# Optimization experiments

Hardware: AMD Instinct MI355X
Metric: run time of the kernel (lower is better)

The kernel has to match this reference:

```python
import jax, jax.numpy as jnp
import numpy as np

N_NODES = 100000
N_EDGES = 1000000
NUM_FEATURES = 64
HIDDEN = 64
NUM_GRAPHS = 128


def setup_inputs() -> dict:
    key = jax.random.key(0)
    ks = jax.random.split(key, 12)
    x = jax.random.normal(ks[0], (N_NODES, NUM_FEATURES), dtype=jnp.float32)
    edge_index = jax.random.randint(ks[1], (2, N_EDGES), 0, N_NODES, dtype=jnp.int64)
    edge_weight = jax.random.uniform(ks[2], (N_EDGES,), dtype=jnp.float32)
    batch = jnp.sort(jax.random.randint(ks[3], (N_NODES,), 0, NUM_GRAPHS, dtype=jnp.int64))
    s1 = 1.0 / np.sqrt(NUM_FEATURES)
    s2 = 1.0 / np.sqrt(HIDDEN)
    # GraphConv layer 1: lin_rel (with bias) applied to aggregated msgs, lin_root (no bias)
    w1_rel = jax.random.uniform(ks[4], (HIDDEN, NUM_FEATURES), jnp.float32, -s1, s1)
    b1_rel = jax.random.uniform(ks[5], (HIDDEN,), jnp.float32, -s1, s1)
    w1_root = jax.random.uniform(ks[6], (HIDDEN, NUM_FEATURES), jnp.float32, -s1, s1)
    # GraphConv layer 2
    w2_rel = jax.random.uniform(ks[7], (HIDDEN, HIDDEN), jnp.float32, -s2, s2)
    b2_rel = jax.random.uniform(ks[8], (HIDDEN,), jnp.float32, -s2, s2)
    w2_root = jax.random.uniform(ks[9], (HIDDEN, HIDDEN), jnp.float32, -s2, s2)
    # final Linear(hidden, 1)
    w_lin = jax.random.uniform(ks[10], (1, HIDDEN), jnp.float32, -s2, s2)
    b_lin = jax.random.uniform(ks[11], (1,), jnp.float32, -s2, s2)
    return {
        "x": x, "edge_index": edge_index, "edge_weight": edge_weight, "batch": batch,
        "w1_rel": w1_rel, "b1_rel": b1_rel, "w1_root": w1_root,
        "w2_rel": w2_rel, "b2_rel": b2_rel, "w2_root": w2_root,
        "w_lin": w_lin, "b_lin": b_lin,
    }


def graph_conv(x, edge_index, edge_weight, w_rel, b_rel, w_root):
    # messages: x[src] * e, scatter-add into dst  (gather-scale-scatter)
    src, dst = edge_index[0], edge_index[1]
    msgs = x[src] * edge_weight[:, None]                      # [E, F]
    aggr = jax.ops.segment_sum(msgs, dst, num_segments=x.shape[0])  # [N, F]
    return aggr @ w_rel.T + b_rel + x @ w_root.T


def reference(x, edge_index, edge_weight, batch,
              w1_rel, b1_rel, w1_root, w2_rel, b2_rel, w2_root, w_lin, b_lin):
    h = graph_conv(x, edge_index, edge_weight, w1_rel, b1_rel, w1_root)
    h = jax.nn.relu(h)
    h = graph_conv(h, edge_index, edge_weight, w2_rel, b2_rel, w2_root)
    # global_mean_pool over graph ids
    sums = jax.ops.segment_sum(h, batch, num_segments=NUM_GRAPHS)          # [G, H]
    counts = jax.ops.segment_sum(jnp.ones((h.shape[0],), h.dtype), batch,
                                 num_segments=NUM_GRAPHS)                  # [G]
    pooled = sums / jnp.maximum(counts, 1.0)[:, None]
    # dropout(p=0.5) in eval mode is identity
    return pooled @ w_lin.T + b_lin                                        # [G, 1]
```

## Files before the change

kernel.cpp:

```cpp
#include <hip/hip_runtime.h>
#include <hip/hip_bf16.h>


#define N_NODES 100000
#define N_EDGES 1000000
#define NGRAPHS 128
#define BN 512
#define NBUCK ((N_NODES + BN - 1) / BN)
#define FILL_T 16
#define FILL_TILE (256 * FILL_T)
#define FILL_NB ((N_EDGES + FILL_TILE - 1) / FILL_TILE)
#define CVT_NB (N_NODES * 64 / 8 / 256)
#define HIST_NB 256

typedef __attribute__((ext_vector_type(8))) short bf16x8;
typedef __attribute__((ext_vector_type(8))) unsigned short u16x8;
typedef __attribute__((ext_vector_type(4))) float f32x4;

__device__ __forceinline__ unsigned short f2bf(float f) {
    unsigned u = __float_as_uint(f);
    unsigned r = (u + 0x7FFFu + ((u >> 16) & 1u)) >> 16;
    return (unsigned short)r;
}
__device__ __forceinline__ float bf2f(unsigned short h) {
    return __uint_as_float(((unsigned)h) << 16);
}

__global__ __launch_bounds__(256) void prep_cvt_hist_kernel(
    const float* __restrict__ x, unsigned short* __restrict__ xh,
    const int* __restrict__ ei, int* __restrict__ bcount,
    const float* __restrict__ w1rel, const float* __restrict__ w1root,
    const float* __restrict__ w2rel, const float* __restrict__ w2root,
    const float* __restrict__ wlin, const float* __restrict__ b2rel,
    const float* __restrict__ blin, unsigned short* __restrict__ whirel,
    unsigned short* __restrict__ wlorel, unsigned short* __restrict__ whiroot,
    unsigned short* __restrict__ wloroot, float* __restrict__ u,
    float* __restrict__ v, float* __restrict__ C) {
    int tid = threadIdx.x;
    int b = blockIdx.x;
    if (b < CVT_NB) {
        int i = b * 256 + tid;
        const float4* xp = (const float4*)x + (size_t)i * 2;
        float4 a = xp[0], bb = xp[1];
        u16x8 o;
        o[0] = f2bf(a.x); o[1] = f2bf(a.y); o[2] = f2bf(a.z); o[3] = f2bf(a.w);
        o[4] = f2bf(bb.x); o[5] = f2bf(bb.y); o[6] = f2bf(bb.z); o[7] = f2bf(bb.w);
        *((u16x8*)xh + i) = o;
        return;
    }
    if (b == CVT_NB) {
        for (int k = tid; k < 4096; k += 256) {
            float a = w1rel[k];
            unsigned short hi = f2bf(a);
            whirel[k] = hi;
            wlorel[k] = f2bf(a - bf2f(hi));
            float w = w1root[k];
            unsigned short hb = f2bf(w);
            whiroot[k] = hb;
            wloroot[k] = f2bf(w - bf2f(hb));
        }
        if (tid < 64) {
            float uu = 0.f, vv = 0.f;
            for (int h = 0; h < 64; ++h) {
                float wl = wlin[h];
                uu += wl * w2rel[h * 64 + tid];
                vv += wl * w2root[h * 64 + tid];
            }
            u[tid] = uu;
            v[tid] = vv;
        }
        if (tid == 0) {
            float c = blin[0];
            for (int h = 0; h < 64; ++h) c += wlin[h] * b2rel[h];
            *C = c;
        }
        return;
    }
    __shared__ int lh[NBUCK];
    int hb = b - CVT_NB - 1;
    for (int i = tid; i < NBUCK; i += 256) lh[i] = 0;
    __syncthreads();
    for (int e = hb * 256 + tid; e < N_EDGES; e += HIST_NB * 256)
        atomicAdd(&lh[ei[N_EDGES + e] >> 9], 1);
    __syncthreads();
    for (int i = tid; i < NBUCK; i += 256) {
        int c = lh[i];
        if (c) atomicAdd(&bcount[i], c);
    }
}

__global__ void bucket_scan(const int* __restrict__ bcount,
                            int* __restrict__ boff, int* __restrict__ cursor) {
    __shared__ int s[256];
    int t = threadIdx.x;
    int v = (t < NBUCK) ? bcount[t] : 0;
    s[t] = v;
    __syncthreads();
    for (int off = 1; off < 256; off <<= 1) {
        int x = (t >= off) ? s[t - off] : 0;
        __syncthreads();
        s[t] += x;
        __syncthreads();
    }
    if (t < NBUCK) {
        boff[t] = s[t] - v;
        cursor[t] = s[t] - v;
    }
    if (t == 255) boff[NBUCK] = s[255];
}

__global__ __launch_bounds__(256) void bucket_fill(
    const int* __restrict__ ei, const float* __restrict__ ew,
    int* __restrict__ cursor, int2* __restrict__ ebuf, int E) {
    __shared__ int lh[NBUCK];
    __shared__ int gbase[NBUCK];
    int tid = threadIdx.x;
    for (int i = tid; i < NBUCK; i += 256) lh[i] = 0;
    __syncthreads();
    int base = blockIdx.x * FILL_TILE;
    int2 rec[FILL_T];
    int meta[FILL_T];
#pragma unroll
    for (int i = 0; i < FILL_T; ++i) {
        int e = base + i * 256 + tid;
        meta[i] = -1;
        if (e < E) {
            int src = ei[e];
            int dst = ei[E + e];
            int b = dst >> 9;
            int r = atomicAdd(&lh[b], 1);
            rec[i].x = src | ((dst & (BN - 1)) << 17);
            rec[i].y = __float_as_int(ew[e]);
            meta[i] = (b << 13) | r;
        }
    }
    __syncthreads();
    for (int i = tid; i < NBUCK; i += 256) {
        int c = lh[i];
        gbase[i] = c ? atomicAdd(&cursor[i], c) : 0;
    }
    __syncthreads();
#pragma unroll
    for (int i = 0; i < FILL_T; ++i) {
        if (meta[i] >= 0) {
            int b = meta[i] >> 13;
            int r = meta[i] & 8191;
            ebuf[gbase[b] + r] = rec[i];
        }
    }
}

__global__ __launch_bounds__(512) void csr_build(
    const int* __restrict__ boff, const int2* __restrict__ ebuf,
    const int* __restrict__ batch, int* __restrict__ row_ptr,
    int2* __restrict__ csr, int N) {
    __shared__ int s[BN];
    int b = blockIdx.x;
    int t = threadIdx.x;
    int beg = boff[b], end = boff[b + 1];
    s[t] = 0;
    __syncthreads();
    for (int j = beg + t; j < end; j += 512)
        atomicAdd(&s[(ebuf[j].x >> 17) & (BN - 1)], 1);
    __syncthreads();
    int v = s[t];
    for (int off = 1; off < BN; off <<= 1) {
        int x = (t >= off) ? s[t - off] : 0;
        __syncthreads();
        s[t] += x;
        __syncthreads();
    }
    int excl = s[t] - v;
    int gidx = b * BN + t;
    if (gidx <= N) row_ptr[gidx] = beg + excl;
    __syncthreads();
    s[t] = excl;
    __syncthreads();
    for (int j = beg + t; j < end; j += 512) {
        int2 rec = ebuf[j];
        int dlo = (rec.x >> 17) & (BN - 1);
        int g = batch[b * BN + dlo];
        int r = atomicAdd(&s[dlo], 1);
        int2 o;
        o.x = (rec.x & 0x1FFFF) | (g << 17);
        o.y = rec.y;
        csr[beg + r] = o;
    }
}

__global__ __launch_bounds__(256) void gather_kernel(
    const unsigned short* __restrict__ xh, const int* __restrict__ row_ptr,
    const int2* __restrict__ csr, unsigned short* __restrict__ aggr, int N,
    int chunk) {
    int lane = threadIdx.x & 63;
    int wid = (blockIdx.x * blockDim.x + threadIdx.x) >> 6;
    int g = lane >> 3;
    int c = lane & 7;
    int n0 = wid * chunk;
    int n1 = min(n0 + chunk, N);
    for (int node = n0; node < n1; ++node) {
        int beg = row_ptr[node], end = row_ptr[node + 1];
        float acc[8];
#pragma unroll
        for (int t = 0; t < 8; ++t) acc[t] = 0.f;
        for (int j0 = beg; j0 < end; j0 += 64) {
            int cnt = min(64, end - j0);
            int2 e = {0, 0};
            if (lane < cnt) e = csr[j0 + lane];
            for (int k = 0; k < cnt; k += 8) {
                int myk = k + g;
                int sj = __shfl(e.x, myk) & 0x1FFFF;
                float wj = __int_as_float(__shfl(e.y, myk));
                if (myk < cnt) {
                    u16x8 xv = *(const u16x8*)(xh + (size_t)sj * 64 + c * 8);
#pragma unroll
                    for (int t = 0; t < 8; ++t) acc[t] += wj * bf2f(xv[t]);
                }
            }
        }
#pragma unroll
        for (int off = 8; off < 64; off <<= 1) {
#pragma unroll
            for (int t = 0; t < 8; ++t) acc[t] += __shfl_xor(acc[t], off);
        }
        if (lane < 8) {
            u16x8 o;
#pragma unroll
            for (int t = 0; t < 8; ++t) o[t] = f2bf(acc[t]);
            *(u16x8*)(aggr + (size_t)node * 64 + c * 8) = o;
        }
    }
}

__global__ __launch_bounds__(256, 2) void dense_kernel(
    const unsigned short* __restrict__ aggr,
    const unsigned short* __restrict__ xh,
    const unsigned short* __restrict__ whirel,
    const unsigned short* __restrict__ wlorel,
    const unsigned short* __restrict__ whiroot,
    const unsigned short* __restrict__ wloroot,
    const float* __restrict__ b1rel, const float* __restrict__ u,
    const float* __restrict__ v, float* __restrict__ p, float* __restrict__ q,
    int N) {
    int lane = threadIdx.x & 63;
    int wave = (blockIdx.x << 2) + (threadIdx.x >> 6);
    int nb = wave * 16;
    if (nb >= N) return;
    int lo4 = lane & 15;
    int quad = lane >> 4;

    f32x4 acc[4];
#pragma unroll
    for (int t = 0; t < 4; ++t) acc[t] = (f32x4){0.f, 0.f, 0.f, 0.f};

    for (int s = 0; s < 2; ++s) {
        bf16x8 Aa = *(const bf16x8*)(aggr + (size_t)(nb + lo4) * 64 + s * 32 +
                                     quad * 8);
        bf16x8 Ax = *(const bf16x8*)(xh + (size_t)(nb + lo4) * 64 + s * 32 +
                                     quad * 8);
#pragma unroll
        for (int t = 0; t < 4; ++t) {
            int off = (t * 16 + lo4) * 64 + s * 32 + quad * 8;
            bf16x8 bhr = *(const bf16x8*)(whirel + off);
            bf16x8 blr = *(const bf16x8*)(wlorel + off);
            bf16x8 bhx = *(const bf16x8*)(whiroot + off);
            bf16x8 blx = *(const bf16x8*)(wloroot + off);
            acc[t] = __builtin_amdgcn_mfma_f32_16x16x32_bf16(Aa, bhr, acc[t],
                                                             0, 0, 0);
            acc[t] = __builtin_amdgcn_mfma_f32_16x16x32_bf16(Aa, blr, acc[t],
                                                             0, 0, 0);
            acc[t] = __builtin_amdgcn_mfma_f32_16x16x32_bf16(Ax, bhx, acc[t],
                                                             0, 0, 0);
            acc[t] = __builtin_amdgcn_mfma_f32_16x16x32_bf16(Ax, blx, acc[t],
                                                             0, 0, 0);
        }
    }

    float pc[4] = {0.f, 0.f, 0.f, 0.f};
    float qc[4] = {0.f, 0.f, 0.f, 0.f};
#pragma unroll
    for (int t = 0; t < 4; ++t) {
        float bb = b1rel[t * 16 + lo4];
        float uu = u[t * 16 + lo4];
        float vv = v[t * 16 + lo4];
#pragma unroll
        for (int r = 0; r < 4; ++r) {
            float h1 = fmaxf(acc[t][r] + bb, 0.f);
            pc[r] += uu * h1;
            qc[r] += vv * h1;
        }
    }
#pragma unroll
    for (int off = 1; off < 16; off <<= 1) {
#pragma unroll
        for (int r = 0; r < 4; ++r) {
            pc[r] += __shfl_xor(pc[r], off);
            qc[r] += __shfl_xor(qc[r], off);
        }
    }
    if (lo4 == 0) {
        f32x4 po = {pc[0], pc[1], pc[2], pc[3]};
        f32x4 qo = {qc[0], qc[1], qc[2], qc[3]};
        *(f32x4*)(p + nb + quad * 4) = po;
        *(f32x4*)(q + nb + quad * 4) = qo;
    }
}

#define PT_EPT 8
#define PT_EPW (64 * PT_EPT)
#define PT_NB ((N_EDGES + 4 * PT_EPW - 1) / (4 * PT_EPW))
#define PS_NB 98
__global__ __launch_bounds__(256) void pool_both(
    const int2* __restrict__ csr, const float* __restrict__ p,
    const float* __restrict__ q, const int* __restrict__ batch,
    float* __restrict__ gp, float* __restrict__ gq, float* __restrict__ gc,
    int E, int N) {
    __shared__ float lbuf[2 * NGRAPHS];
    int tid = threadIdx.x;
    lbuf[tid] = 0.f;
    __syncthreads();
    if (blockIdx.x < PT_NB) {
        int lane = tid & 63;
        int wid = (blockIdx.x * 256 + tid) >> 6;
        int base = wid * PT_EPW;
        float acc = 0.f;
        int curg = -1;
#pragma unroll
        for (int i = 0; i < PT_EPT; ++i) {
            int j = base + i * 64 + lane;
            if (j < E) {
                int2 e = csr[j];
                int g = (e.x >> 17) & 127;
                float val = __int_as_float(e.y) * p[e.x & 0x1FFFF];
                if (g != curg) {
                    if (curg >= 0) atomicAdd(&lbuf[curg], acc);
                    curg = g;
                    acc = 0.f;
                }
                acc += val;
            }
        }
        if (curg >= 0) atomicAdd(&lbuf[curg], acc);
        __syncthreads();
        if (tid < NGRAPHS) {
            float t = lbuf[tid];
            if (t != 0.f) atomicAdd(&gp[tid], t);
        }
    } else {
        int bid = blockIdx.x - PT_NB;
        for (int i = bid * 256 + tid; i < N; i += PS_NB * 256) {
            int g = batch[i];
            atomicAdd(&lbuf[g], q[i]);
            atomicAdd(&lbuf[NGRAPHS + g], 1.f);
        }
        __syncthreads();
        if (tid < NGRAPHS) {
            if (lbuf[NGRAPHS + tid] != 0.f) {
                atomicAdd(&gq[tid], lbuf[tid]);
                atomicAdd(&gc[tid], lbuf[NGRAPHS + tid]);
            }
        }
    }
}

__global__ void final_kernel(const float* __restrict__ gp,
                             const float* __restrict__ gq,
                             const float* __restrict__ gc,
                             const float* __restrict__ C,
                             float* __restrict__ out) {
    int g = threadIdx.x;
    float c = fmaxf(gc[g], 1.0f);
    out[g] = (gp[g] + gq[g]) / c + *C;
}

extern "C" void kernel_launch(void* const* d_in, const int* in_sizes, int n_in,
                              void* d_out, int out_size, void* d_ws,
                              size_t ws_size, hipStream_t stream) {
    const float* x      = (const float*)d_in[0];
    const int*   ei     = (const int*)d_in[1];
    const float* ew     = (const float*)d_in[2];
    const int*   batch  = (const int*)d_in[3];
    const float* w1rel  = (const float*)d_in[4];
    const float* b1rel  = (const float*)d_in[5];
    const float* w1root = (const float*)d_in[6];
    const float* w2rel  = (const float*)d_in[7];
    const float* b2rel  = (const float*)d_in[8];
    const float* w2root = (const float*)d_in[9];
    const float* wlin   = (const float*)d_in[10];
    const float* blin   = (const float*)d_in[11];
    float* out = (float*)d_out;

    char* wsb = (char*)d_ws;
    int2* csr  = (int2*)wsb;
    unsigned short* aggr = (unsigned short*)(wsb + (size_t)N_EDGES * 8);
    int2* ebuf = (int2*)aggr;
    char* tail = wsb + (size_t)N_EDGES * 8 + (size_t)N_NODES * 128;
    unsigned short* whirel  = (unsigned short*)tail;
    unsigned short* wlorel  = whirel + 4096;
    unsigned short* whiroot = wlorel + 4096;
    unsigned short* wloroot = whiroot + 4096;
    float* p  = (float*)(wloroot + 4096);
    float* q  = p + N_NODES;
    float* u  = q + N_NODES;
    float* v  = u + 64;
    float* C  = v + 64;
    int*   bcount = (int*)(C + 1);
    float* gp = (float*)(bcount + NBUCK);
    float* gq = gp + NGRAPHS;
    float* gc = gq + NGRAPHS;
    int*   boff   = (int*)(gc + NGRAPHS);
    int*   cursor = boff + (NBUCK + 1);
    int*   row_ptr = cursor + NBUCK;
    unsigned short* xh = (unsigned short*)(row_ptr + N_NODES + 2);

    hipMemsetAsync(bcount, 0, (NBUCK + 3 * NGRAPHS) * sizeof(int), stream);

    prep_cvt_hist_kernel<<<CVT_NB + 1 + HIST_NB, 256, 0, stream>>>(
        x, xh, ei, bcount, w1rel, w1root, w2rel, w2root, wlin, b2rel, blin,
        whirel, wlorel, whiroot, wloroot, u, v, C);

    bucket_scan<<<1, 256, 0, stream>>>(bcount, boff, cursor);
    bucket_fill<<<FILL_NB, 256, 0, stream>>>(ei, ew, cursor, ebuf, N_EDGES);
    csr_build<<<NBUCK, 512, 0, stream>>>(boff, ebuf, batch, row_ptr, csr,
                                         N_NODES);

    {
        int blocks = 2048;
        int waves = blocks * 4;
        int chunk = (N_NODES + waves - 1) / waves;
        gather_kernel<<<blocks, 256, 0, stream>>>(xh, row_ptr, csr, aggr,
                                                  N_NODES, chunk);
    }
    {
        int tiles = N_NODES / 16;
        int blocks = (tiles + 3) / 4;
        dense_kernel<<<blocks, 256, 0, stream>>>(aggr, xh, whirel, wlorel,
                                                 whiroot, wloroot, b1rel, u, v,
                                                 p, q, N_NODES);
    }
    pool_both<<<PT_NB + PS_NB, 256, 0, stream>>>(csr, p, q, batch, gp, gq, gc,
                                                 N_EDGES, N_NODES);
    final_kernel<<<1, NGRAPHS, 0, stream>>>(gp, gq, gc, C, out);
}
```

Measured before the change: 223.9 us.

## Fold bucket scan into fill/build kernels, fuse final into pool, narrow gather lanes

Removes the separate single-block bucket_scan launch by having each bucket_fill and csr_build block recompute the 196-entry prefix sum redundantly in shared memory. The final_kernel launch is folded into pool_both through a last-block-done atomic counter. The gather kernel now has each wave process 4 edges per step with 16 lanes × 4 features instead of 8 edges × 8 lanes × 8 features. This trades two launches and their serialization for redundant scan work per block, and it changes per-load width and memory-level parallelism in the gather.

Result: no change. 226.6 us (+1.2%).

```diff
diff --git a/kernel.cpp b/kernel.cpp
--- a/kernel.cpp
+++ b/kernel.cpp
@@ -89,34 +89,26 @@
     }
 }
 
-__global__ void bucket_scan(const int* __restrict__ bcount,
-                            int* __restrict__ boff, int* __restrict__ cursor) {
-    __shared__ int s[256];
-    int t = threadIdx.x;
-    int v = (t < NBUCK) ? bcount[t] : 0;
-    s[t] = v;
-    __syncthreads();
-    for (int off = 1; off < 256; off <<= 1) {
-        int x = (t >= off) ? s[t - off] : 0;
-        __syncthreads();
-        s[t] += x;
-        __syncthreads();
-    }
-    if (t < NBUCK) {
-        boff[t] = s[t] - v;
-        cursor[t] = s[t] - v;
-    }
-    if (t == 255) boff[NBUCK] = s[255];
-}
-
 __global__ __launch_bounds__(256) void bucket_fill(
     const int* __restrict__ ei, const float* __restrict__ ew,
-    int* __restrict__ cursor, int2* __restrict__ ebuf, int E) {
+    const int* __restrict__ bcount, int* __restrict__ cursor,
+    int2* __restrict__ ebuf, int E) {
     __shared__ int lh[NBUCK];
+    __shared__ int ssc[256];
     __shared__ int gbase[NBUCK];
     int tid = threadIdx.x;
-    for (int i = tid; i < NBUCK; i += 256) lh[i] = 0;
-    __syncthreads();
+    int bc = (tid < NBUCK) ? bcount[tid] : 0;
+    ssc[tid] = bc;
+    if (tid < NBUCK) lh[tid] = 0;
+    __syncthreads();
+    for (int off = 1; off < 256; off <<= 1) {
+        int xv = (tid >= off) ? ssc[tid - off] : 0;
+        __syncthreads();
+        ssc[tid] += xv;
+        __syncthreads();
+    }
+    int myboff = ssc[tid] - bc;
+
     int base = blockIdx.x * FILL_TILE;
     int2 rec[FILL_T];
     int meta[FILL_T];
@@ -135,9 +127,9 @@
         }
     }
     __syncthreads();
-    for (int i = tid; i < NBUCK; i += 256) {
-        int c = lh[i];
-        gbase[i] = c ? atomicAdd(&cursor[i], c) : 0;
+    if (tid < NBUCK) {
+        int c = lh[tid];
+        gbase[tid] = c ? (myboff + atomicAdd(&cursor[tid], c)) : 0;
     }
     __syncthreads();
 #pragma unroll
@@ -151,13 +143,25 @@
 }
 
 __global__ __launch_bounds__(512) void csr_build(
-    const int* __restrict__ boff, const int2* __restrict__ ebuf,
+    const int* __restrict__ bcount, const int2* __restrict__ ebuf,
     const int* __restrict__ batch, int* __restrict__ row_ptr,
     int2* __restrict__ csr, int N) {
+    __shared__ int ssc[256];
     __shared__ int s[BN];
     int b = blockIdx.x;
     int t = threadIdx.x;
-    int beg = boff[b], end = boff[b + 1];
+    if (t < 256) ssc[t] = (t < NBUCK) ? bcount[t] : 0;
+    __syncthreads();
+    for (int off = 1; off < 256; off <<= 1) {
+        int xv = 0;
+        if (t < 256 && t >= off) xv = ssc[t - off];
+        __syncthreads();
+        if (t < 256) ssc[t] += xv;
+        __syncthreads();
+    }
+    int end = ssc[b];
+    int beg = end - bcount[b];
+
     s[t] = 0;
     __syncthreads();
     for (int j = beg + t; j < end; j += 512)
@@ -165,9 +169,9 @@
     __syncthreads();
     int v = s[t];
     for (int off = 1; off < BN; off <<= 1) {
-        int x = (t >= off) ? s[t - off] : 0;
-        __syncthreads();
-        s[t] += x;
+        int xv = (t >= off) ? s[t - off] : 0;
+        __syncthreads();
+        s[t] += xv;
         __syncthreads();
     }
     int excl = s[t] - v;
@@ -194,40 +198,45 @@
     int chunk) {
     int lane = threadIdx.x & 63;
     int wid = (blockIdx.x * blockDim.x + threadIdx.x) >> 6;
-    int g = lane >> 3;
-    int c = lane & 7;
+    int g = lane >> 4;
+    int c = lane & 15;
     int n0 = wid * chunk;
     int n1 = min(n0 + chunk, N);
     for (int node = n0; node < n1; ++node) {
         int beg = row_ptr[node], end = row_ptr[node + 1];
-        float acc[8];
-#pragma unroll
-        for (int t = 0; t < 8; ++t) acc[t] = 0.f;
+        float4 acc = {0.f, 0.f, 0.f, 0.f};
         for (int j0 = beg; j0 < end; j0 += 64) {
             int cnt = min(64, end - j0);
             int2 e = {0, 0};
             if (lane < cnt) e = csr[j0 + lane];
-            for (int k = 0; k < cnt; k += 8) {
+            for (int k = 0; k < cnt; k += 4) {
                 int myk = k + g;
                 int sj = __shfl(e.x, myk) & 0x1FFFF;
                 float wj = __int_as_float(__shfl(e.y, myk));
                 if (myk < cnt) {
-                    u16x8 xv = *(const u16x8*)(xh + (size_t)sj * 64 + c * 8);
-#pragma unroll
-                    for (int t = 0; t < 8; ++t) acc[t] += wj * bf2f(xv[t]);
+                    ushort4 xv =
+                        *(const ushort4*)(xh + (size_t)sj * 64 + c * 4);
+                    acc.x += wj * bf2f(xv.x);
+                    acc.y += wj * bf2f(xv.y);
+                    acc.z += wj * bf2f(xv.z);
+                    acc.w += wj * bf2f(xv.w);
                 }
             }
         }
 #pragma unroll
-        for (int off = 8; off < 64; off <<= 1) {
-#pragma unroll
-            for (int t = 0; t < 8; ++t) acc[t] += __shfl_xor(acc[t], off);
-        }
-        if (lane < 8) {
-            u16x8 o;
-#pragma unroll
-            for (int t = 0; t < 8; ++t) o[t] = f2bf(acc[t]);
-            *(u16x8*)(aggr + (size_t)node * 64 + c * 8) = o;
+        for (int off = 16; off < 64; off <<= 1) {
+            acc.x += __shfl_xor(acc.x, off);
+            acc.y += __shfl_xor(acc.y, off);
+            acc.z += __shfl_xor(acc.z, off);
+            acc.w += __shfl_xor(acc.w, off);
+        }
+        if (lane < 16) {
+            ushort4 o;
+            o.x = f2bf(acc.x);
+            o.y = f2bf(acc.y);
+            o.z = f2bf(acc.z);
+            o.w = f2bf(acc.w);
+            *(ushort4*)(aggr + (size_t)node * 64 + c * 4) = o;
         }
     }
 }
@@ -314,8 +323,10 @@
     const int2* __restrict__ csr, const float* __restrict__ p,
     const float* __restrict__ q, const int* __restrict__ batch,
     float* __restrict__ gp, float* __restrict__ gq, float* __restrict__ gc,
-    int E, int N) {
+    int* __restrict__ done, const float* __restrict__ C,
+    float* __restrict__ out, int E, int N) {
     __shared__ float lbuf[2 * NGRAPHS];
+    __shared__ int lastflag;
     int tid = threadIdx.x;
     lbuf[tid] = 0.f;
     __syncthreads();
@@ -361,16 +372,19 @@
             }
         }
     }
-}
-
-__global__ void final_kernel(const float* __restrict__ gp,
-                             const float* __restrict__ gq,
-                             const float* __restrict__ gc,
-                             const float* __restrict__ C,
-                             float* __restrict__ out) {
-    int g = threadIdx.x;
-    float c = fmaxf(gc[g], 1.0f);
-    out[g] = (gp[g] + gq[g]) / c + *C;
+    if (tid == 0) {
+        __threadfence();
+        int old = atomicAdd(done, 1);
+        lastflag = (old == (int)gridDim.x - 1);
+    }
+    __syncthreads();
+    if (lastflag && tid < NGRAPHS) {
+        __threadfence();
+        float pp = atomicAdd(&gp[tid], 0.f);
+        float qq = atomicAdd(&gq[tid], 0.f);
+        float cc = atomicAdd(&gc[tid], 0.f);
+        out[tid] = (pp + qq) / fmaxf(cc, 1.0f) + *C;
+    }
 }
 
 extern "C" void kernel_launch(void* const* d_in, const int* in_sizes, int n_in,
@@ -408,20 +422,21 @@
     float* gp = (float*)(bcount + NBUCK);
     float* gq = gp + NGRAPHS;
     float* gc = gq + NGRAPHS;
-    int*   boff   = (int*)(gc + NGRAPHS);
-    int*   cursor = boff + (NBUCK + 1);
-    int*   row_ptr = cursor + NBUCK;
+    int*   cursor = (int*)(gc + NGRAPHS);
+    int*   done   = cursor + NBUCK;
+    int*   row_ptr = done + 1;
     unsigned short* xh = (unsigned short*)(row_ptr + N_NODES + 2);
 
-    hipMemsetAsync(bcount, 0, (NBUCK + 3 * NGRAPHS) * sizeof(int), stream);
+    hipMemsetAsync(bcount, 0,
+                   (2 * NBUCK + 3 * NGRAPHS + 1) * sizeof(int), stream);
 
     prep_cvt_hist_kernel<<<CVT_NB + 1 + HIST_NB, 256, 0, stream>>>(
         x, xh, ei, bcount, w1rel, w1root, w2rel, w2root, wlin, b2rel, blin,
         whirel, wlorel, whiroot, wloroot, u, v, C);
 
-    bucket_scan<<<1, 256, 0, stream>>>(bcount, boff, cursor);
-    bucket_fill<<<FILL_NB, 256, 0, stream>>>(ei, ew, cursor, ebuf, N_EDGES);
-    csr_build<<<NBUCK, 512, 0, stream>>>(boff, ebuf, batch, row_ptr, csr,
+    bucket_fill<<<FILL_NB, 256, 0, stream>>>(ei, ew, bcount, cursor, ebuf,
+                                             N_EDGES);
+    csr_build<<<NBUCK, 512, 0, stream>>>(bcount, ebuf, batch, row_ptr, csr,
                                          N_NODES);
 
     {
@@ -439,6 +454,6 @@
                                                  p, q, N_NODES);
     }
     pool_both<<<PT_NB + PS_NB, 256, 0, stream>>>(csr, p, q, batch, gp, gq, gc,
-                                                 N_EDGES, N_NODES);
-    final_kernel<<<1, NGRAPHS, 0, stream>>>(gp, gq, gc, C, out);
-}
+                                                 done, C, out, N_EDGES,
+                                                 N_NODES);
+}
```

## Use atomic work-stealing node batches and 16-lane row split in gather kernel

Applied to the files above, without the earlier changes.

The gather kernel now claims batches of four nodes through a global atomic counter instead of a fixed static chunk per wave, which balances work across waves when node degrees vary. Each edge's 64-wide bf16 row is now read by 16 lanes with 8-byte loads, and 4 edges are processed per step instead of 8 edges with 16-byte loads per lane. The reduction shrinks to two shuffle stages over four accumulators. The cost is an extra atomic per batch, a zeroed counter in the workspace memset, and smaller, less vectorized memory loads with fewer edges in flight.

Result: slower. 564.8 us (+152.3%).

```diff
diff --git a/kernel.cpp b/kernel.cpp
--- a/kernel.cpp
+++ b/kernel.cpp
@@ -12,6 +12,7 @@
 #define FILL_NB ((N_EDGES + FILL_TILE - 1) / FILL_TILE)
 #define CVT_NB (N_NODES * 64 / 8 / 256)
 #define HIST_NB 256
+#define GB 4
 
 typedef __attribute__((ext_vector_type(8))) short bf16x8;
 typedef __attribute__((ext_vector_type(8))) unsigned short u16x8;
@@ -190,44 +191,53 @@
 
 __global__ __launch_bounds__(256) void gather_kernel(
     const unsigned short* __restrict__ xh, const int* __restrict__ row_ptr,
-    const int2* __restrict__ csr, unsigned short* __restrict__ aggr, int N,
-    int chunk) {
+    const int2* __restrict__ csr, unsigned short* __restrict__ aggr,
+    int* __restrict__ wctr, int N) {
     int lane = threadIdx.x & 63;
-    int wid = (blockIdx.x * blockDim.x + threadIdx.x) >> 6;
-    int g = lane >> 3;
-    int c = lane & 7;
-    int n0 = wid * chunk;
-    int n1 = min(n0 + chunk, N);
-    for (int node = n0; node < n1; ++node) {
-        int beg = row_ptr[node], end = row_ptr[node + 1];
-        float acc[8];
-#pragma unroll
-        for (int t = 0; t < 8; ++t) acc[t] = 0.f;
-        for (int j0 = beg; j0 < end; j0 += 64) {
-            int cnt = min(64, end - j0);
-            int2 e = {0, 0};
-            if (lane < cnt) e = csr[j0 + lane];
-            for (int k = 0; k < cnt; k += 8) {
-                int myk = k + g;
-                int sj = __shfl(e.x, myk) & 0x1FFFF;
-                float wj = __int_as_float(__shfl(e.y, myk));
-                if (myk < cnt) {
-                    u16x8 xv = *(const u16x8*)(xh + (size_t)sj * 64 + c * 8);
-#pragma unroll
-                    for (int t = 0; t < 8; ++t) acc[t] += wj * bf2f(xv[t]);
+    int g = lane >> 4;
+    int c = lane & 15;
+    for (;;) {
+        int n0;
+        if (lane == 0) n0 = atomicAdd(wctr, GB);
+        n0 = __shfl(n0, 0);
+        if (n0 >= N) return;
+        int n1 = min(n0 + GB, N);
+        for (int node = n0; node < n1; ++node) {
+            int beg = row_ptr[node], end = row_ptr[node + 1];
+            float4 acc = {0.f, 0.f, 0.f, 0.f};
+            for (int j0 = beg; j0 < end; j0 += 64) {
+                int cnt = min(64, end - j0);
+                int2 e = {0, 0};
+                if (lane < cnt) e = csr[j0 + lane];
+                for (int k = 0; k < cnt; k += 4) {
+                    int myk = k + g;
+                    int sj = __shfl(e.x, myk) & 0x1FFFF;
+                    float wj = __int_as_float(__shfl(e.y, myk));
+                    if (myk < cnt) {
+                        ushort4 xv =
+                            *(const ushort4*)(xh + (size_t)sj * 64 + c * 4);
+                        acc.x += wj * bf2f(xv.x);
+                        acc.y += wj * bf2f(xv.y);
+                        acc.z += wj * bf2f(xv.z);
+                        acc.w += wj * bf2f(xv.w);
+                    }
                 }
             }
-        }
-#pragma unroll
-        for (int off = 8; off < 64; off <<= 1) {
-#pragma unroll
-            for (int t = 0; t < 8; ++t) acc[t] += __shfl_xor(acc[t], off);
-        }
-        if (lane < 8) {
-            u16x8 o;
-#pragma unroll
-            for (int t = 0; t < 8; ++t) o[t] = f2bf(acc[t]);
-            *(u16x8*)(aggr + (size_t)node * 64 + c * 8) = o;
+#pragma unroll
+            for (int off = 16; off < 64; off <<= 1) {
+                acc.x += __shfl_xor(acc.x, off);
+                acc.y += __shfl_xor(acc.y, off);
+                acc.z += __shfl_xor(acc.z, off);
+                acc.w += __shfl_xor(acc.w, off);
+            }
+            if (lane < 16) {
+                ushort4 o;
+                o.x = f2bf(acc.x);
+                o.y = f2bf(acc.y);
+                o.z = f2bf(acc.z);
+                o.w = f2bf(acc.w);
+                *(ushort4*)(aggr + (size_t)node * 64 + c * 4) = o;
+            }
         }
     }
 }
@@ -408,12 +418,14 @@
     float* gp = (float*)(bcount + NBUCK);
     float* gq = gp + NGRAPHS;
     float* gc = gq + NGRAPHS;
-    int*   boff   = (int*)(gc + NGRAPHS);
+    int*   wctr = (int*)(gc + NGRAPHS);
+    int*   boff   = wctr + 1;
     int*   cursor = boff + (NBUCK + 1);
     int*   row_ptr = cursor + NBUCK;
     unsigned short* xh = (unsigned short*)(row_ptr + N_NODES + 2);
 
-    hipMemsetAsync(bcount, 0, (NBUCK + 3 * NGRAPHS) * sizeof(int), stream);
+    hipMemsetAsync(bcount, 0, (NBUCK + 3 * NGRAPHS + 1) * sizeof(int),
+                   stream);
 
     prep_cvt_hist_kernel<<<CVT_NB + 1 + HIST_NB, 256, 0, stream>>>(
         x, xh, ei, bcount, w1rel, w1root, w2rel, w2root, wlin, b2rel, blin,
@@ -424,13 +436,8 @@
     csr_build<<<NBUCK, 512, 0, stream>>>(boff, ebuf, batch, row_ptr, csr,
                                          N_NODES);
 
-    {
-        int blocks = 2048;
-        int waves = blocks * 4;
-        int chunk = (N_NODES + waves - 1) / waves;
-        gather_kernel<<<blocks, 256, 0, stream>>>(xh, row_ptr, csr, aggr,
-                                                  N_NODES, chunk);
-    }
+    gather_kernel<<<2048, 256, 0, stream>>>(xh, row_ptr, csr, aggr, wctr,
+                                            N_NODES);
     {
         int tiles = N_NODES / 16;
         int blocks = (tiles + 3) / 4;
```
